# Kernel tuning notes

Measured on AMD Instinct MI355X. Metric: run time of the kernel, lower is better.

The kernel has to match this reference:

```python
import jax, jax.numpy as jnp
import numpy as np

DIM = 256
HEADS = 8
WSZ = (2, 7, 7)
SSZ = (1, 3, 3)
EPS = 1e-5


def _rel_index(wsz):
    wt, wh, ww = wsz
    coords = np.stack(np.meshgrid(np.arange(wt), np.arange(wh), np.arange(ww), indexing='ij'))
    coords = coords.reshape(3, -1)  # (3, N)
    rel = coords[:, :, None] - coords[:, None, :]  # (3, N, N)
    rel = rel.transpose(1, 2, 0).copy()  # (N, N, 3)
    rel[:, :, 0] += wt - 1
    rel[:, :, 1] += wh - 1
    rel[:, :, 2] += ww - 1
    rel[:, :, 0] *= (2 * wh - 1) * (2 * ww - 1)
    rel[:, :, 1] *= (2 * ww - 1)
    return rel.sum(-1)  # (N, N) int


def _attn_mask_np(T, H, W, wsz, ssz):
    wt, wh, ww = wsz
    st, sh, sw = ssz
    img = np.zeros((T, H, W), np.int32)
    cnt = 0
    for t in (slice(0, -wt), slice(-wt, -st), slice(-st, None)):
        for h in (slice(0, -wh), slice(-wh, -sh), slice(-sh, None)):
            for w in (slice(0, -ww), slice(-ww, -sw), slice(-sw, None)):
                img[t, h, w] = cnt
                cnt += 1
    m = img.reshape(T // wt, wt, H // wh, wh, W // ww, ww)
    m = m.transpose(0, 2, 4, 1, 3, 5).reshape(-1, wt * wh * ww)  # (nW, N)
    diff = m[:, :, None] - m[:, None, :]
    return np.where(diff != 0, -100.0, 0.0).astype(np.float32)  # (nW, N, N)


def _ln(x, w, b):
    mu = x.mean(-1, keepdims=True)
    var = jnp.mean((x - mu) ** 2, -1, keepdims=True)
    return (x - mu) * jax.lax.rsqrt(var + EPS) * w + b


def _window_partition(x, wsz):
    B, T, H, W, C = x.shape
    wt, wh, ww = wsz
    x = x.reshape(B, T // wt, wt, H // wh, wh, W // ww, ww, C)
    x = x.transpose(0, 1, 3, 5, 2, 4, 6, 7)
    return x.reshape(-1, wt * wh * ww, C)


def _window_reverse(xw, wsz, B, T, H, W):
    wt, wh, ww = wsz
    C = xw.shape[-1]
    x = xw.reshape(B, T // wt, H // wh, W // ww, wt, wh, ww, C)
    x = x.transpose(0, 1, 4, 2, 5, 3, 6, 7)
    return x.reshape(B, T, H, W, C)


def setup_inputs() -> dict:
    key = jax.random.key(0)
    ks = jax.random.split(key, 8)
    B, T, H, W = 2, 8, 56, 56
    d = DIM
    hid = 4 * d
    rpe_rows = (2 * WSZ[0] - 1) * (2 * WSZ[1] - 1) * (2 * WSZ[2] - 1)
    s = 0.02
    return {
        'x': jax.random.normal(ks[0], (B, T, H, W, d), jnp.float32),
        'norm1_w': jnp.ones((d,), jnp.float32),
        'norm1_b': jnp.zeros((d,), jnp.float32),
        'qkv_w': jax.random.normal(ks[1], (3 * d, d), jnp.float32) * s,
        'qkv_b': jnp.zeros((3 * d,), jnp.float32),
        'proj_w': jax.random.normal(ks[2], (d, d), jnp.float32) * s,
        'proj_b': jnp.zeros((d,), jnp.float32),
        'rpe_table': jax.random.normal(ks[3], (rpe_rows, HEADS), jnp.float32) * s,
        'norm2_w': jnp.ones((d,), jnp.float32),
        'norm2_b': jnp.zeros((d,), jnp.float32),
        'fc1_w': jax.random.normal(ks[4], (hid, d), jnp.float32) * s,
        'fc1_b': jnp.zeros((hid,), jnp.float32),
        'fc2_w': jax.random.normal(ks[5], (d, hid), jnp.float32) * s,
        'fc2_b': jnp.zeros((d,), jnp.float32),
    }


def reference(x, norm1_w, norm1_b, qkv_w, qkv_b, proj_w, proj_b, rpe_table,
              norm2_w, norm2_b, fc1_w, fc1_b, fc2_w, fc2_b):
    B, T, H, W, C = x.shape
    wt, wh, ww = WSZ
    N = wt * wh * ww
    hd = C // HEADS
    scale = hd ** -0.5

    shortcut = x
    h = _ln(x, norm1_w, norm1_b)
    # shifted branch: cyclic roll + mask
    h = jnp.roll(h, (-SSZ[0], -SSZ[1], -SSZ[2]), axis=(1, 2, 3))
    mask = jnp.asarray(_attn_mask_np(T, H, W, WSZ, SSZ))  # (nW, N, N)
    nW = mask.shape[0]

    xw = _window_partition(h, WSZ)  # (B*nW, N, C)
    Bw = xw.shape[0]

    qkv = xw @ qkv_w.T + qkv_b  # (Bw, N, 3C)
    qkv = qkv.reshape(Bw, N, 3, HEADS, hd).transpose(2, 0, 3, 1, 4)
    q, k, v = qkv[0], qkv[1], qkv[2]  # (Bw, H, N, hd)

    idx = _rel_index(WSZ)  # (N, N)
    bias = rpe_table[idx].transpose(2, 0, 1)  # (heads, N, N)

    attn = jnp.einsum('bhnd,bhmd->bhnm', q * scale, k) + bias[None]
    attn = attn.reshape(B, nW, HEADS, N, N) + mask[None, :, None]
    attn = jax.nn.softmax(attn, axis=-1).reshape(Bw, HEADS, N, N)

    out = jnp.einsum('bhnm,bhmd->bhnd', attn, v)
    out = out.transpose(0, 2, 1, 3).reshape(Bw, N, C)
    out = out @ proj_w.T + proj_b

    out = _window_reverse(out, WSZ, B, T, H, W)
    out = jnp.roll(out, (SSZ[0], SSZ[1], SSZ[2]), axis=(1, 2, 3))

    x = shortcut + out
    h2 = _ln(x, norm2_w, norm2_b)
    h2 = jax.nn.gelu(h2 @ fc1_w.T + fc1_b, approximate=False)
    h2 = h2 @ fc2_w.T + fc2_b
    return x + h2
```

## Files before the change

kernel.cpp:

```cpp
#include <hip/hip_runtime.h>
#include <math.h>

#define TOKENS 50176
#define NWIN   512
#define C_DIM  256

typedef __attribute__((ext_vector_type(8))) short short8;
typedef __attribute__((ext_vector_type(4))) float f32x4;

__device__ __forceinline__ unsigned short f2bf(float f) {
    unsigned int u = __builtin_bit_cast(unsigned int, f);
    u += 0x7fffu + ((u >> 16) & 1);
    return (unsigned short)(u >> 16);
}

__device__ __forceinline__ void gll16(const void* g, void* l) {
    __builtin_amdgcn_global_load_lds(
        (const __attribute__((address_space(1))) unsigned int*)g,
        (__attribute__((address_space(3))) unsigned int*)l, 16, 0, 0);
}

__device__ __forceinline__ int win_token_to_flat(int u) {
    int g = u / 98;
    int n = u - g * 98;
    int bb  = g >> 8;
    int rem = g & 255;
    int tb = rem >> 6, hb = (rem >> 3) & 7, wb = rem & 7;
    int dt = n / 49;
    int r2 = n - dt * 49;
    int dh = r2 / 7, dw = r2 - dh * 7;
    int t = tb * 2 + dt, h = hb * 7 + dh, w = wb * 7 + dw;
    int ts = (t + 1) & 7;
    int hs = h + 3; if (hs >= 56) hs -= 56;
    int wsx = w + 3; if (wsx >= 56) wsx -= 56;
    return ((bb * 8 + ts) * 56 + hs) * 56 + wsx;
}

__global__ __launch_bounds__(256) void cvt_kernel(
        const float* __restrict__ src, unsigned short* __restrict__ dst, int n) {
    int i = blockIdx.x * 256 + threadIdx.x;
    if (i < n) dst[i] = f2bf(src[i]);
}

__global__ __launch_bounds__(256) void bm_kernel(
        const float* __restrict__ rpe, float* __restrict__ bm) {
    int i = blockIdx.x * 256 + threadIdx.x;
    int c  = i % 112;
    int t1 = i / 112;
    int r  = t1 % 112;
    int t2 = t1 / 112;
    int head = t2 & 7;
    int cls  = t2 >> 3;
    float val;
    if (c >= 98) {
        val = -1e30f;
    } else if (r >= 98) {
        val = 0.f;
    } else {
        int dt = r / 49, rr = r - dt * 49, dh = rr / 7, dw = rr - dh * 7;
        int dt2 = c / 49, cc = c - dt2 * 49, dh2 = cc / 7, dw2 = cc - dh2 * 7;
        int rt  = (cls & 4) ? (dt  == 0 ? 1 : 2) : 0;
        int rh  = (cls & 2) ? (dh  <  4 ? 1 : 2) : 0;
        int rw  = (cls & 1) ? (dw  <  4 ? 1 : 2) : 0;
        int rt2 = (cls & 4) ? (dt2 == 0 ? 1 : 2) : 0;
        int rh2 = (cls & 2) ? (dh2 <  4 ? 1 : 2) : 0;
        int rw2 = (cls & 1) ? (dw2 <  4 ? 1 : 2) : 0;
        int reg1 = rt * 9 + rh * 3 + rw, reg2 = rt2 * 9 + rh2 * 3 + rw2;
        int idx = (dt - dt2 + 1) * 169 + (dh - dh2 + 6) * 13 + (dw - dw2 + 6);
        val = rpe[idx * 8 + head] + ((reg1 == reg2) ? 0.f : -100.f);
    }
    bm[i] = val;
}

template<bool GATHER>
__global__ __launch_bounds__(256) void ln_kernel(
        const float* __restrict__ x, const float* __restrict__ w,
        const float* __restrict__ b, unsigned short* __restrict__ out) {
    int token = blockIdx.x * 4 + (threadIdx.x >> 6);
    int lane  = threadIdx.x & 63;
    size_t so = GATHER ? (size_t)win_token_to_flat(token) * C_DIM
                       : (size_t)token * C_DIM;
    const float* src = x + so;
    float v[4];
    float sum = 0.f;
#pragma unroll
    for (int j = 0; j < 4; ++j) { v[j] = src[lane + 64 * j]; sum += v[j]; }
#pragma unroll
    for (int o = 32; o > 0; o >>= 1) sum += __shfl_xor(sum, o, 64);
    float mu = sum * (1.f / 256.f);
    float var = 0.f;
#pragma unroll
    for (int j = 0; j < 4; ++j) { float d = v[j] - mu; var += d * d; }
#pragma unroll
    for (int o = 32; o > 0; o >>= 1) var += __shfl_xor(var, o, 64);
    float rstd = rsqrtf(var * (1.f / 256.f) + 1e-5f);
    unsigned short* dst = out + (size_t)token * C_DIM;
#pragma unroll
    for (int j = 0; j < 4; ++j) {
        int c = lane + 64 * j;
        dst[c] = f2bf((v[j] - mu) * rstd * w[c] + b[c]);
    }
}

template<int EPI>
__global__ __launch_bounds__(256) void mfma_gemm(
        const unsigned short* __restrict__ A, const unsigned short* __restrict__ B,
        const float* __restrict__ bias, const float* __restrict__ res,
        void* __restrict__ Cout, int M, int N, int K) {
    __shared__ __attribute__((aligned(16))) unsigned short Asm[128 * 32];
    __shared__ __attribute__((aligned(16))) unsigned short Bsm[128 * 32];
    int tid = threadIdx.x;
    int wave = tid >> 6, lane = tid & 63;
    int row0 = blockIdx.y * 128, col0 = blockIdx.x * 128;
    int wr = (wave >> 1) * 64;
    int wc = (wave & 1) * 64;

    f32x4 acc[4][4] = {};

    int sr = tid >> 2;
    int sk = (tid & 3) * 8;
    const unsigned short* Ag0 = A + (size_t)(row0 + sr) * K + sk;
    const unsigned short* Ag1 = A + (size_t)(row0 + 64 + sr) * K + sk;
    const unsigned short* Bg0 = B + (size_t)(col0 + sr) * K + sk;
    const unsigned short* Bg1 = B + (size_t)(col0 + 64 + sr) * K + sk;
    unsigned short* Al = Asm + tid * 8;
    unsigned short* Bl = Bsm + tid * 8;

    int fm = lane & 15, fk = (lane >> 4) * 8;

    for (int k0 = 0; k0 < K; k0 += 32) {
        __syncthreads();
        gll16(Ag0 + k0, Al);
        gll16(Ag1 + k0, Al + 64 * 32);
        gll16(Bg0 + k0, Bl);
        gll16(Bg1 + k0, Bl + 64 * 32);
        __syncthreads();
        short8 af[4], bf[4];
#pragma unroll
        for (int t4 = 0; t4 < 4; ++t4) {
            af[t4] = *(const short8*)&Asm[(wr + t4 * 16 + fm) * 32 + fk];
            bf[t4] = *(const short8*)&Bsm[(wc + t4 * 16 + fm) * 32 + fk];
        }
#pragma unroll
        for (int i = 0; i < 4; ++i)
#pragma unroll
            for (int j = 0; j < 4; ++j)
                acc[i][j] = __builtin_amdgcn_mfma_f32_16x16x32_bf16(
                    af[i], bf[j], acc[i][j], 0, 0, 0);
    }

    int crow0 = row0 + wr + (lane >> 4) * 4;
    int ccol0 = col0 + wc + (lane & 15);
    float bj[4];
#pragma unroll
    for (int j = 0; j < 4; ++j) bj[j] = bias[ccol0 + j * 16];

    if (EPI == 0) {
        unsigned short* C = (unsigned short*)Cout;
        float mul = (col0 < 256) ? 0.17677669529663687f : 1.f;
#pragma unroll
        for (int i = 0; i < 4; ++i)
#pragma unroll
            for (int v = 0; v < 4; ++v) {
                size_t base = (size_t)(crow0 + i * 16 + v) * N + ccol0;
#pragma unroll
                for (int j = 0; j < 4; ++j)
                    C[base + j * 16] = f2bf((acc[i][j][v] + bj[j]) * mul);
            }
    } else if (EPI == 1) {
        float* C = (float*)Cout;
#pragma unroll
        for (int i = 0; i < 4; ++i)
#pragma unroll
            for (int v = 0; v < 4; ++v) {
                int r = crow0 + i * 16 + v;
                size_t base = (size_t)win_token_to_flat(r) * C_DIM + ccol0;
#pragma unroll
                for (int j = 0; j < 4; ++j)
                    C[base + j * 16] = res[base + j * 16] + acc[i][j][v] + bj[j];
            }
    } else if (EPI == 2) {
        unsigned short* C = (unsigned short*)Cout;
#pragma unroll
        for (int i = 0; i < 4; ++i)
#pragma unroll
            for (int v = 0; v < 4; ++v) {
                size_t base = (size_t)(crow0 + i * 16 + v) * N + ccol0;
#pragma unroll
                for (int j = 0; j < 4; ++j) {
                    float val = acc[i][j][v] + bj[j];
                    C[base + j * 16] =
                        f2bf(0.5f * val * (1.f + erff(val * 0.70710678118654752f)));
                }
            }
    } else {
        float* C = (float*)Cout;
#pragma unroll
        for (int i = 0; i < 4; ++i)
#pragma unroll
            for (int v = 0; v < 4; ++v) {
                size_t base = (size_t)(crow0 + i * 16 + v) * N + ccol0;
#pragma unroll
                for (int j = 0; j < 4; ++j)
                    C[base + j * 16] = res[base + j * 16] + acc[i][j][v] + bj[j];
            }
    }
}

__global__ __launch_bounds__(256) void attn_mfma_kernel(
        const unsigned short* __restrict__ qkv, const float* __restrict__ bm,
        unsigned short* __restrict__ out) {
    __shared__ __attribute__((aligned(16))) unsigned short Vt[32][136];
    __shared__ __attribute__((aligned(16))) unsigned short Pw[4][16][136];
    int blk = blockIdx.x;
    int g = blk >> 3, head = blk & 7;
    int tid = threadIdx.x, wave = tid >> 6, lane = tid & 63;

    for (int i = tid; i < 32 * 30; i += 256) {
        int d = i / 30, c = 98 + (i - d * 30);
        Vt[d][c] = 0;
    }
    const unsigned short* vbase = qkv + (size_t)g * 98 * 768 + 512 + head * 32;
    for (int i = tid; i < 98 * 16; i += 256) {
        int n = i >> 4, dp = i & 15;
        unsigned int val = *(const unsigned int*)(vbase + (size_t)n * 768 + dp * 2);
        Vt[dp * 2][n]     = (unsigned short)val;
        Vt[dp * 2 + 1][n] = (unsigned short)(val >> 16);
    }
    {
        int m = lane >> 2, c = 112 + (lane & 3) * 4;
        *(unsigned long long*)&Pw[wave][m][c] = 0ULL;
    }
    __syncthreads();

    const unsigned short* qbase = qkv + (size_t)g * 98 * 768 + head * 32;
    const unsigned short* kbase = qbase + 256;
    int rem = g & 255;
    int cls = (((rem >> 6) == 3) << 2) | (((((rem >> 3) & 7)) == 7) << 1) | ((rem & 7) == 7);
    const float* bmh = bm + (size_t)(cls * 8 + head) * 112 * 112;

    int fm = lane & 15, fq = lane >> 4;
    int fk = fq * 8;
    unsigned short* obase = out + (size_t)g * 98 * 256 + head * 32;

    for (int s = wave; s < 7; s += 4) {
        int m0 = s * 16;
        int arow = m0 + fm; if (arow > 97) arow = 97;
        short8 af = *(const short8*)(qbase + (size_t)arow * 768 + fk);
        f32x4 S[7];
        f32x4 z = {0.f, 0.f, 0.f, 0.f};
#pragma unroll
        for (int j = 0; j < 7; ++j) {
            int krow = j * 16 + fm; if (krow > 97) krow = 97;
            short8 kf = *(const short8*)(kbase + (size_t)krow * 768 + fk);
            S[j] = __builtin_amdgcn_mfma_f32_16x16x32_bf16(af, kf, z, 0, 0, 0);
        }
        const float* bmrow = bmh + (m0 + fq * 4) * 112 + fm;
#pragma unroll
        for (int j = 0; j < 7; ++j)
#pragma unroll
            for (int v = 0; v < 4; ++v)
                S[j][v] += bmrow[v * 112 + j * 16];
        float inv[4];
#pragma unroll
        for (int v = 0; v < 4; ++v) {
            float m_ = S[0][v];
#pragma unroll
            for (int j = 1; j < 7; ++j) m_ = fmaxf(m_, S[j][v]);
#pragma unroll
            for (int o = 1; o < 16; o <<= 1) m_ = fmaxf(m_, __shfl_xor(m_, o, 64));
            float t = 0.f;
#pragma unroll
            for (int j = 0; j < 7; ++j) { S[j][v] = __expf(S[j][v] - m_); t += S[j][v]; }
#pragma unroll
            for (int o = 1; o < 16; o <<= 1) t += __shfl_xor(t, o, 64);
            inv[v] = 1.f / t;
        }
#pragma unroll
        for (int j = 0; j < 7; ++j)
#pragma unroll
            for (int v = 0; v < 4; ++v)
                Pw[wave][fq * 4 + v][j * 16 + fm] = f2bf(S[j][v]);
        f32x4 O0 = {0.f, 0.f, 0.f, 0.f}, O1 = {0.f, 0.f, 0.f, 0.f};
#pragma unroll
        for (int ks = 0; ks < 4; ++ks) {
            short8 pf = *(const short8*)&Pw[wave][fm][ks * 32 + fk];
            short8 v0 = *(const short8*)&Vt[fm][ks * 32 + fk];
            short8 v1 = *(const short8*)&Vt[16 + fm][ks * 32 + fk];
            O0 = __builtin_amdgcn_mfma_f32_16x16x32_bf16(pf, v0, O0, 0, 0, 0);
            O1 = __builtin_amdgcn_mfma_f32_16x16x32_bf16(pf, v1, O1, 0, 0, 0);
        }
#pragma unroll
        for (int v = 0; v < 4; ++v) {
            int row = m0 + fq * 4 + v;
            if (row < 98) {
                obase[(size_t)row * 256 + fm]      = f2bf(O0[v] * inv[v]);
                obase[(size_t)row * 256 + 16 + fm] = f2bf(O1[v] * inv[v]);
            }
        }
    }
}

extern "C" void kernel_launch(void* const* d_in, const int* in_sizes, int n_in,
                              void* d_out, int out_size, void* d_ws, size_t ws_size,
                              hipStream_t stream) {
    const float* x     = (const float*)d_in[0];
    const float* n1w   = (const float*)d_in[1];
    const float* n1b   = (const float*)d_in[2];
    const float* qkvw  = (const float*)d_in[3];
    const float* qkvb  = (const float*)d_in[4];
    const float* projw = (const float*)d_in[5];
    const float* projb = (const float*)d_in[6];
    const float* rpe   = (const float*)d_in[7];
    const float* n2w   = (const float*)d_in[8];
    const float* n2b   = (const float*)d_in[9];
    const float* fc1w  = (const float*)d_in[10];
    const float* fc1b  = (const float*)d_in[11];
    const float* fc2w  = (const float*)d_in[12];
    const float* fc2b  = (const float*)d_in[13];
    float* out = (float*)d_out;

    unsigned short* wqkv  = (unsigned short*)d_ws;
    unsigned short* wproj = wqkv + 768 * 256;
    unsigned short* wfc1  = wproj + 256 * 256;
    unsigned short* wfc2  = wfc1 + 1024 * 256;
    float* bm = (float*)(wfc2 + 256 * 1024);
    unsigned short* actA  = (unsigned short*)(bm + 8 * 8 * 112 * 112);
    unsigned short* attnO = actA + (size_t)TOKENS * 256;
    unsigned short* qkv_bf = attnO + (size_t)TOKENS * 256;
    unsigned short* fc1o = qkv_bf;

    bm_kernel<<<8 * 8 * 112 * 112 / 256, 256, 0, stream>>>(rpe, bm);
    cvt_kernel<<<(768 * 256 + 255) / 256, 256, 0, stream>>>(qkvw, wqkv, 768 * 256);
    cvt_kernel<<<(256 * 256 + 255) / 256, 256, 0, stream>>>(projw, wproj, 256 * 256);
    cvt_kernel<<<(1024 * 256 + 255) / 256, 256, 0, stream>>>(fc1w, wfc1, 1024 * 256);
    cvt_kernel<<<(256 * 1024 + 255) / 256, 256, 0, stream>>>(fc2w, wfc2, 256 * 1024);

    ln_kernel<true><<<TOKENS / 4, 256, 0, stream>>>(x, n1w, n1b, actA);
    mfma_gemm<0><<<dim3(768 / 128, TOKENS / 128), 256, 0, stream>>>(
        actA, wqkv, qkvb, nullptr, qkv_bf, TOKENS, 768, 256);
    attn_mfma_kernel<<<NWIN * 8, 256, 0, stream>>>(qkv_bf, bm, attnO);
    mfma_gemm<1><<<dim3(256 / 128, TOKENS / 128), 256, 0, stream>>>(
        attnO, wproj, projb, x, out, TOKENS, 256, 256);
    ln_kernel<false><<<TOKENS / 4, 256, 0, stream>>>(out, n2w, n2b, actA);
    mfma_gemm<2><<<dim3(1024 / 128, TOKENS / 128), 256, 0, stream>>>(
        actA, wfc1, fc1b, nullptr, fc1o, TOKENS, 1024, 256);
    mfma_gemm<3><<<dim3(256 / 128, TOKENS / 128), 256, 0, stream>>>(
        fc1o, wfc2, fc2b, out, out, TOKENS, 256, 1024);
}
```

Baseline: 412.2 us.

## Double-buffer GEMM LDS tiles with XOR swizzle and grouped block ordering

The bf16 MFMA GEMM now keeps two LDS buffers, so the next K-slice is loaded with global_load_lds while the current slice feeds the MFMAs. This halves the barriers per iteration and lets memory latency overlap with compute. It also XOR-swizzles the 16-byte column chunk per row group on both the global load and the fragment read, to reduce LDS bank conflicts. Finally, it remaps block IDs into 8 interleaved groups to change L2 locality. The cost is double the LDS use, which may lower occupancy. Correctness also depends on the async LDS loads being complete at the single barrier.

```diff
diff --git a/kernel.cpp b/kernel.cpp
--- a/kernel.cpp
+++ b/kernel.cpp
@@ -107,46 +107,61 @@
         const unsigned short* __restrict__ A, const unsigned short* __restrict__ B,
         const float* __restrict__ bias, const float* __restrict__ res,
         void* __restrict__ Cout, int M, int N, int K) {
-    __shared__ __attribute__((aligned(16))) unsigned short Asm[128 * 32];
-    __shared__ __attribute__((aligned(16))) unsigned short Bsm[128 * 32];
+    __shared__ __attribute__((aligned(16))) unsigned short Asm[2][128 * 32];
+    __shared__ __attribute__((aligned(16))) unsigned short Bsm[2][128 * 32];
     int tid = threadIdx.x;
     int wave = tid >> 6, lane = tid & 63;
-    int row0 = blockIdx.y * 128, col0 = blockIdx.x * 128;
+
+    int nwg = gridDim.x * gridDim.y;
+    int bid = blockIdx.y * gridDim.x + blockIdx.x;
+    int swz = (bid & 7) * (nwg >> 3) + (bid >> 3);
+    int bx = swz % gridDim.x, by = swz / gridDim.x;
+
+    int row0 = by * 128, col0 = bx * 128;
     int wr = (wave >> 1) * 64;
     int wc = (wave & 1) * 64;
 
     f32x4 acc[4][4] = {};
 
     int sr = tid >> 2;
-    int sk = (tid & 3) * 8;
+    int sk = (((tid & 3) ^ ((sr >> 2) & 3)) * 8);
     const unsigned short* Ag0 = A + (size_t)(row0 + sr) * K + sk;
     const unsigned short* Ag1 = A + (size_t)(row0 + 64 + sr) * K + sk;
     const unsigned short* Bg0 = B + (size_t)(col0 + sr) * K + sk;
     const unsigned short* Bg1 = B + (size_t)(col0 + 64 + sr) * K + sk;
-    unsigned short* Al = Asm + tid * 8;
-    unsigned short* Bl = Bsm + tid * 8;
-
-    int fm = lane & 15, fk = (lane >> 4) * 8;
-
-    for (int k0 = 0; k0 < K; k0 += 32) {
+    int loff = tid * 8;
+
+    int fm = lane & 15, fq = lane >> 4;
+    int fks = (fq ^ ((fm >> 2) & 3)) * 8;
+
+    gll16(Ag0, &Asm[0][loff]);
+    gll16(Ag1, &Asm[0][loff + 2048]);
+    gll16(Bg0, &Bsm[0][loff]);
+    gll16(Bg1, &Bsm[0][loff + 2048]);
+
+    int nk = K >> 5;
+    for (int s = 0; s < nk; ++s) {
+        int cur = s & 1;
         __syncthreads();
-        gll16(Ag0 + k0, Al);
-        gll16(Ag1 + k0, Al + 64 * 32);
-        gll16(Bg0 + k0, Bl);
-        gll16(Bg1 + k0, Bl + 64 * 32);
-        __syncthreads();
-        short8 af[4], bf[4];
+        if (s + 1 < nk) {
+            int k0 = (s + 1) << 5;
+            gll16(Ag0 + k0, &Asm[cur ^ 1][loff]);
+            gll16(Ag1 + k0, &Asm[cur ^ 1][loff + 2048]);
+            gll16(Bg0 + k0, &Bsm[cur ^ 1][loff]);
+            gll16(Bg1 + k0, &Bsm[cur ^ 1][loff + 2048]);
+        }
+        short8 af[4], bfr[4];
 #pragma unroll
         for (int t4 = 0; t4 < 4; ++t4) {
-            af[t4] = *(const short8*)&Asm[(wr + t4 * 16 + fm) * 32 + fk];
-            bf[t4] = *(const short8*)&Bsm[(wc + t4 * 16 + fm) * 32 + fk];
+            af[t4]  = *(const short8*)&Asm[cur][(wr + t4 * 16 + fm) * 32 + fks];
+            bfr[t4] = *(const short8*)&Bsm[cur][(wc + t4 * 16 + fm) * 32 + fks];
         }
 #pragma unroll
         for (int i = 0; i < 4; ++i)
 #pragma unroll
             for (int j = 0; j < 4; ++j)
                 acc[i][j] = __builtin_amdgcn_mfma_f32_16x16x32_bf16(
-                    af[i], bf[j], acc[i][j], 0, 0, 0);
+                    af[i], bfr[j], acc[i][j], 0, 0, 0);
     }
 
     int crow0 = row0 + wr + (lane >> 4) * 4;
```

New measurement: 391.7 us. 5.0% less time.
